# Kernel optimization log

Measured on AMD Instinct MI355X. Metric: run time of the kernel, lower is better.

## Reference

```python
import jax, jax.numpy as jnp
import numpy as np

FILTS = 100  # conv padding = aconv_filts
SCALING = 2.0


def setup_inputs() -> dict:
    key = jax.random.key(0)
    ks = jax.random.split(key, 9)
    T, DUNITS, ATT, EPROJ, CH, K = 50000, 1024, 512, 512, 10, 2 * FILTS + 1
    return {
        "dec_z": jax.random.normal(ks[0], (1, DUNITS), jnp.float32),
        "att_prev": jax.random.uniform(ks[1], (1, T), jnp.float32),
        "pre_compute_enc_h": jax.random.normal(ks[2], (1, T, ATT), jnp.float32),
        "enc_h": jax.random.normal(ks[3], (1, T, EPROJ), jnp.float32),
        "mask": jnp.zeros((1, T), jnp.float32),
        "conv_w": jax.random.normal(ks[4], (CH, 1, K), jnp.float32) * 0.05,
        "w_att": jax.random.normal(ks[5], (ATT, CH), jnp.float32) * 0.05,
        "w_dec": jax.random.normal(ks[6], (ATT, DUNITS), jnp.float32) * 0.02,
        "w_gvec": jax.random.normal(ks[7], (1, ATT), jnp.float32) * 0.05,
        "b_gvec": jnp.zeros((1,), jnp.float32),
    }


def reference(dec_z, att_prev, pre_compute_enc_h, enc_h, mask, conv_w, w_att, w_dec, w_gvec, b_gvec):
    # loc_conv: 1-channel 1D conv over previous attention weights -> [1, CH, T]
    att_conv = jax.lax.conv_general_dilated(
        att_prev[:, None, :], conv_w, window_strides=(1,),
        padding=[(FILTS, FILTS)], dimension_numbers=("NCH", "OIH", "NCH"))
    # mlp_att: [1, T, ATT]
    att_conv = jnp.einsum("bct,ac->bta", att_conv, w_att)
    # mlp_dec, tiled over frames: [1, 1, ATT]
    dec_tiled = (dec_z @ w_dec.T)[:, None, :]
    # gvec(tanh(...)) -> scores e: [1, T]
    e = jnp.einsum("bta,a->bt", jnp.tanh(att_conv + pre_compute_enc_h + dec_tiled), w_gvec[0]) + b_gvec
    e = e + mask
    w = jax.nn.softmax(SCALING * e, axis=1)  # [1, T]
    c = jnp.sum(enc_h * w[..., None], axis=1)  # [1, EPROJ]
    return (c, w)
```

## Files before the change

kernel.cpp:

```cpp
#include <hip/hip_runtime.h>
#include <math.h>


constexpr int ATT    = 512;
constexpr int CH     = 10;
constexpr int KW     = 201;
constexpr int FILTS  = 100;
constexpr int DUNITS = 1024;
constexpr int NB1    = 1024;
constexpr int NB3    = 256;
constexpr float SCALING = 2.0f;

__device__ __forceinline__ float wave_reduce_sum(float v) {
    #pragma unroll
    for (int off = 32; off > 0; off >>= 1) v += __shfl_xor(v, off, 64);
    return v;
}

__device__ __forceinline__ float fast_tanh(float x) {
    x = fminf(fmaxf(x, -15.f), 15.f);
    float e = __expf(2.f * x);
    return __fdividef(e - 1.f, e + 1.f);
}

__global__ __launch_bounds__(256, 4) void k0_conv_dec(
    const float* __restrict__ att_prev,
    const float* __restrict__ conv_w,
    const float* __restrict__ dec_z,
    const float* __restrict__ w_dec,
    float* __restrict__ ws_aconv,
    float* __restrict__ ws_dec,
    int T, int nbconv)
{
    if ((int)blockIdx.x < nbconv) {
        __shared__ float s_ap[256 + KW - 1];
        __shared__ float s_w[CH * KW];
        const int t0 = blockIdx.x * 256;
        for (int i = threadIdx.x; i < 256 + KW - 1; i += 256) {
            int t = t0 - FILTS + i;
            s_ap[i] = (t >= 0 && t < T) ? att_prev[t] : 0.f;
        }
        for (int i = threadIdx.x; i < CH * KW; i += 256) s_w[i] = conv_w[i];
        __syncthreads();
        const int t = t0 + threadIdx.x;
        if (t < T) {
            float acc[CH];
            #pragma unroll
            for (int c = 0; c < CH; ++c) acc[c] = 0.f;
            for (int k = 0; k < KW; ++k) {
                float x = s_ap[threadIdx.x + k];
                #pragma unroll
                for (int c = 0; c < CH; ++c) acc[c] += x * s_w[c * KW + k];
            }
            #pragma unroll
            for (int c = 0; c < CH; ++c) ws_aconv[t * CH + c] = acc[c];
        }
    } else {
        const int b    = blockIdx.x - nbconv;
        const int wid  = threadIdx.x >> 6;
        const int lane = threadIdx.x & 63;
        const int a    = b * 4 + wid;
        const float4* wd = (const float4*)(w_dec + a * DUNITS);
        const float4* dz = (const float4*)dec_z;
        float acc = 0.f;
        #pragma unroll
        for (int q = 0; q < 4; ++q) {
            float4 wv = wd[lane + q * 64];
            float4 zv = dz[lane + q * 64];
            acc += wv.x * zv.x + wv.y * zv.y + wv.z * zv.z + wv.w * zv.w;
        }
        acc = wave_reduce_sum(acc);
        if (lane == 0) ws_dec[a] = acc;
    }
}

__global__ __launch_bounds__(256, 3) void k1_scores(
    const float* __restrict__ pre,
    const float* __restrict__ mask,
    const float* __restrict__ w_att,
    const float* __restrict__ w_gvec,
    const float* __restrict__ b_gvec,
    const float* __restrict__ ws_dec,
    const float* __restrict__ ws_aconv,
    float* __restrict__ ws_e,
    float* __restrict__ ws_ms,
    int T)
{
    __shared__ float s_watt[ATT * CH];
    __shared__ float s_m[4], s_s[4];
    for (int i = threadIdx.x; i < ATT * CH; i += 256) s_watt[i] = w_att[i];
    __syncthreads();

    const int wid  = threadIdx.x >> 6;
    const int lane = threadIdx.x & 63;

    float wa[8][CH];
    #pragma unroll
    for (int j = 0; j < 4; ++j) {
        #pragma unroll
        for (int c = 0; c < CH; ++c) {
            wa[j][c]     = s_watt[(lane * 4 + j) * CH + c];
            wa[4 + j][c] = s_watt[(256 + lane * 4 + j) * CH + c];
        }
    }
    const float4 dlo = ((const float4*)ws_dec)[lane];
    const float4 dhi = ((const float4*)ws_dec)[64 + lane];
    const float4 glo = ((const float4*)w_gvec)[lane];
    const float4 ghi = ((const float4*)w_gvec)[64 + lane];
    const float  bg  = b_gvec[0];

    float m = -INFINITY, s = 0.f;
    const float4* pre4 = (const float4*)pre;
    const int gw = blockIdx.x * 4 + wid;

    for (int tb = gw * 4; tb < T; tb += NB1 * 4 * 4) {
        float4 p0[4], p1[4];
        #pragma unroll
        for (int i = 0; i < 4; ++i) {
            int t = tb + i;
            if (t < T) {
                p0[i] = pre4[t * 128 + lane];
                p1[i] = pre4[t * 128 + 64 + lane];
            }
        }
        #pragma unroll
        for (int i = 0; i < 4; ++i) {
            int t = tb + i;
            if (t >= T) break;
            float ac[CH];
            #pragma unroll
            for (int c = 0; c < CH; ++c) ac[c] = ws_aconv[t * CH + c];
            float av[8];
            #pragma unroll
            for (int j = 0; j < 8; ++j) {
                float v = 0.f;
                #pragma unroll
                for (int c = 0; c < CH; ++c) v += ac[c] * wa[j][c];
                av[j] = v;
            }
            float x0 = fast_tanh(p0[i].x + dlo.x + av[0]);
            float x1 = fast_tanh(p0[i].y + dlo.y + av[1]);
            float x2 = fast_tanh(p0[i].z + dlo.z + av[2]);
            float x3 = fast_tanh(p0[i].w + dlo.w + av[3]);
            float x4 = fast_tanh(p1[i].x + dhi.x + av[4]);
            float x5 = fast_tanh(p1[i].y + dhi.y + av[5]);
            float x6 = fast_tanh(p1[i].z + dhi.z + av[6]);
            float x7 = fast_tanh(p1[i].w + dhi.w + av[7]);
            float acc = glo.x * x0 + glo.y * x1 + glo.z * x2 + glo.w * x3
                      + ghi.x * x4 + ghi.y * x5 + ghi.z * x6 + ghi.w * x7;
            acc = wave_reduce_sum(acc);
            float y = SCALING * (acc + bg + mask[t]);
            if (lane == 0) ws_e[t] = y;
            float nm = fmaxf(m, y);
            s = s * __expf(m - nm) + __expf(y - nm);
            m = nm;
        }
    }
    if (lane == 0) { s_m[wid] = m; s_s[wid] = s; }
    __syncthreads();
    if (threadIdx.x == 0) {
        float M = s_m[0], S = s_s[0];
        #pragma unroll
        for (int w = 1; w < 4; ++w) {
            float m2 = s_m[w], s2 = s_s[w];
            float nm = fmaxf(M, m2);
            S = S * __expf(M - nm) + s2 * __expf(m2 - nm);
            M = nm;
        }
        ws_ms[blockIdx.x * 2]     = M;
        ws_ms[blockIdx.x * 2 + 1] = S;
    }
}

__global__ __launch_bounds__(256, 4) void k2_merge(
    const float* __restrict__ ws_ms, float* __restrict__ ws_glob,
    float* __restrict__ out, int nb)
{
    __shared__ float s_m[256], s_s[256];
    float m = -INFINITY, s = 0.f;
    for (int i = threadIdx.x; i < nb; i += 256) {
        float m2 = ws_ms[i * 2], s2 = ws_ms[i * 2 + 1];
        float nm = fmaxf(m, m2);
        s = s * __expf(m - nm) + s2 * __expf(m2 - nm);
        m = nm;
    }
    s_m[threadIdx.x] = m; s_s[threadIdx.x] = s;
    __syncthreads();
    for (int off = 128; off > 0; off >>= 1) {
        if ((int)threadIdx.x < off) {
            float M = s_m[threadIdx.x], S = s_s[threadIdx.x];
            float m2 = s_m[threadIdx.x + off], s2 = s_s[threadIdx.x + off];
            float nm = fmaxf(M, m2);
            s_s[threadIdx.x] = S * __expf(M - nm) + s2 * __expf(m2 - nm);
            s_m[threadIdx.x] = nm;
        }
        __syncthreads();
    }
    if (threadIdx.x == 0) { ws_glob[0] = s_m[0]; ws_glob[1] = 1.f / s_s[0]; }
    out[threadIdx.x]       = 0.f;
    out[threadIdx.x + 256] = 0.f;
}

__global__ __launch_bounds__(256, 4) void k3_ctx(
    const float* __restrict__ enc_h,
    const float* __restrict__ ws_e,
    const float* __restrict__ ws_glob,
    float* __restrict__ out,
    float* __restrict__ ws_c,
    int T)
{
    const int wid  = threadIdx.x >> 6;
    const int lane = threadIdx.x & 63;
    const float M  = ws_glob[0];
    const float IS = ws_glob[1];
    const float4* eh4 = (const float4*)enc_h;

    float4 a0 = make_float4(0.f, 0.f, 0.f, 0.f);
    float4 a1 = make_float4(0.f, 0.f, 0.f, 0.f);
    const int gw = blockIdx.x * 4 + wid;

    for (int tb = gw * 8; tb < T; tb += NB3 * 4 * 8) {
        float4 e0[8], e1[8];
        float  y[8];
        #pragma unroll
        for (int i = 0; i < 8; ++i) {
            int t = tb + i;
            if (t < T) {
                e0[i] = eh4[t * 128 + lane];
                e1[i] = eh4[t * 128 + 64 + lane];
                y[i]  = ws_e[t];
            }
        }
        #pragma unroll
        for (int i = 0; i < 8; ++i) {
            int t = tb + i;
            if (t >= T) break;
            float w = __expf(y[i] - M) * IS;
            if (lane == 0) out[ATT + t] = w;
            a0.x += w * e0[i].x; a0.y += w * e0[i].y;
            a0.z += w * e0[i].z; a0.w += w * e0[i].w;
            a1.x += w * e1[i].x; a1.y += w * e1[i].y;
            a1.z += w * e1[i].z; a1.w += w * e1[i].w;
        }
    }

    __shared__ float4 s_c[4 * 128];
    s_c[wid * 128 + lane]      = a0;
    s_c[wid * 128 + 64 + lane] = a1;
    __syncthreads();
    const float* sc = (const float*)s_c;
    for (int a = threadIdx.x; a < ATT; a += 256) {
        float v = sc[a] + sc[512 + a] + sc[1024 + a] + sc[1536 + a];
        ws_c[blockIdx.x * ATT + a] = v;
    }
}

__global__ __launch_bounds__(256, 4) void k4_reduce(
    const float* __restrict__ ws_c, float* __restrict__ out)
{
    const int gt  = blockIdx.x * 256 + threadIdx.x;
    const int a   = gt & (ATT - 1);
    const int grp = gt >> 9;
    float v = 0.f;
    #pragma unroll
    for (int i = 0; i < 8; ++i) v += ws_c[(grp * 8 + i) * ATT + a];
    atomicAdd(&out[a], v);
}

extern "C" void kernel_launch(void* const* d_in, const int* in_sizes, int n_in,
                              void* d_out, int out_size, void* d_ws, size_t ws_size,
                              hipStream_t stream)
{
    const float* dec_z    = (const float*)d_in[0];
    const float* att_prev = (const float*)d_in[1];
    const float* pre      = (const float*)d_in[2];
    const float* enc_h    = (const float*)d_in[3];
    const float* mask     = (const float*)d_in[4];
    const float* conv_w   = (const float*)d_in[5];
    const float* w_att    = (const float*)d_in[6];
    const float* w_dec    = (const float*)d_in[7];
    const float* w_gvec   = (const float*)d_in[8];
    const float* b_gvec   = (const float*)d_in[9];
    const int T = in_sizes[1];

    float* ws       = (float*)d_ws;
    float* ws_dec   = ws;
    float* ws_aconv = ws_dec + ATT;
    float* ws_e     = ws_aconv + (size_t)T * CH;
    float* ws_ms    = ws_e + T;
    float* ws_glob  = ws_ms + NB1 * 2;
    float* ws_c     = ws_glob + 4;
    float* out      = (float*)d_out;

    const int nbconv = (T + 255) / 256;

    hipLaunchKernelGGL(k0_conv_dec, dim3(nbconv + ATT / 4), dim3(256), 0, stream,
                       att_prev, conv_w, dec_z, w_dec, ws_aconv, ws_dec, T, nbconv);
    hipLaunchKernelGGL(k1_scores, dim3(NB1), dim3(256), 0, stream,
                       pre, mask, w_att, w_gvec, b_gvec, ws_dec, ws_aconv,
                       ws_e, ws_ms, T);
    hipLaunchKernelGGL(k2_merge, dim3(1), dim3(256), 0, stream,
                       ws_ms, ws_glob, out, NB1);
    hipLaunchKernelGGL(k3_ctx, dim3(NB3), dim3(256), 0, stream,
                       enc_h, ws_e, ws_glob, out, ws_c, T);
    hipLaunchKernelGGL(k4_reduce, dim3(64), dim3(256), 0, stream,
                       ws_c, out);
}
```

Measured before the change: 276.1 us.

## Fold softmax merge and context reduction into ctx kernel, restructure conv

Removes the separate single-block merge kernel by having every ctx block redo the 1024-partial max/sum merge itself. It also drops the final reduce kernel and atomically adds per-block context sums straight into the output. The conv kernel now uses 64-frame tiles, splits the filter taps across four waves and reduces through shared memory. Conv outputs are padded to 12 channels so the scores kernel can load them as float4. The changes cut launch count and serial single-block latency, in exchange for redundant merge work per block and more atomics.

```diff
diff --git a/kernel.cpp b/kernel.cpp
--- a/kernel.cpp
+++ b/kernel.cpp
@@ -4,11 +4,13 @@
 
 constexpr int ATT    = 512;
 constexpr int CH     = 10;
+constexpr int PCH    = 12;
 constexpr int KW     = 201;
 constexpr int FILTS  = 100;
 constexpr int DUNITS = 1024;
 constexpr int NB1    = 1024;
-constexpr int NB3    = 256;
+constexpr int NB3    = 1024;
+constexpr int CT     = 64;
 constexpr float SCALING = 2.0f;
 
 __device__ __forceinline__ float wave_reduce_sum(float v) {
@@ -30,37 +32,59 @@
     const float* __restrict__ w_dec,
     float* __restrict__ ws_aconv,
     float* __restrict__ ws_dec,
+    float* __restrict__ out,
     int T, int nbconv)
 {
     if ((int)blockIdx.x < nbconv) {
-        __shared__ float s_ap[256 + KW - 1];
-        __shared__ float s_w[CH * KW];
-        const int t0 = blockIdx.x * 256;
-        for (int i = threadIdx.x; i < 256 + KW - 1; i += 256) {
+        __shared__ float s_ap[CT + KW - 1];
+        __shared__ float s_wt[KW * 12];
+        __shared__ float s_part[4 * CT * CH];
+        const int t0 = blockIdx.x * CT;
+        for (int i = threadIdx.x; i < CT + KW - 1; i += 256) {
             int t = t0 - FILTS + i;
             s_ap[i] = (t >= 0 && t < T) ? att_prev[t] : 0.f;
         }
-        for (int i = threadIdx.x; i < CH * KW; i += 256) s_w[i] = conv_w[i];
+        for (int i = threadIdx.x; i < CH * KW; i += 256) {
+            int c = i % CH, k = i / CH;
+            s_wt[k * 12 + c] = conv_w[c * KW + k];
+        }
         __syncthreads();
-        const int t = t0 + threadIdx.x;
-        if (t < T) {
-            float acc[CH];
-            #pragma unroll
-            for (int c = 0; c < CH; ++c) acc[c] = 0.f;
-            for (int k = 0; k < KW; ++k) {
-                float x = s_ap[threadIdx.x + k];
-                #pragma unroll
-                for (int c = 0; c < CH; ++c) acc[c] += x * s_w[c * KW + k];
-            }
-            #pragma unroll
-            for (int c = 0; c < CH; ++c) ws_aconv[t * CH + c] = acc[c];
+        const int tl = threadIdx.x & 63;
+        const int kq = threadIdx.x >> 6;
+        float acc[CH];
+        #pragma unroll
+        for (int c = 0; c < CH; ++c) acc[c] = 0.f;
+        for (int k = kq; k < KW; k += 4) {
+            float x = s_ap[tl + k];
+            const float4 w0 = *(const float4*)&s_wt[k * 12];
+            const float4 w1 = *(const float4*)&s_wt[k * 12 + 4];
+            const float2 w2 = *(const float2*)&s_wt[k * 12 + 8];
+            acc[0] += x * w0.x; acc[1] += x * w0.y;
+            acc[2] += x * w0.z; acc[3] += x * w0.w;
+            acc[4] += x * w1.x; acc[5] += x * w1.y;
+            acc[6] += x * w1.z; acc[7] += x * w1.w;
+            acc[8] += x * w2.x; acc[9] += x * w2.y;
+        }
+        #pragma unroll
+        for (int c = 0; c < CH; ++c) s_part[kq * (CT * CH) + tl * CH + c] = acc[c];
+        __syncthreads();
+        for (int idx = threadIdx.x; idx < CT * PCH; idx += 256) {
+            int t = idx / PCH, c = idx % PCH;
+            float v = 0.f;
+            if (c < CH) {
+                int j = t * CH + c;
+                v = s_part[j] + s_part[CT * CH + j]
+                  + s_part[2 * CT * CH + j] + s_part[3 * CT * CH + j];
+            }
+            if (t0 + t < T) ws_aconv[(size_t)(t0 + t) * PCH + c] = v;
         }
     } else {
         const int b    = blockIdx.x - nbconv;
         const int wid  = threadIdx.x >> 6;
         const int lane = threadIdx.x & 63;
         const int a    = b * 4 + wid;
-        const float4* wd = (const float4*)(w_dec + a * DUNITS);
+        if (threadIdx.x < 4) out[b * 4 + threadIdx.x] = 0.f;
+        const float4* wd = (const float4*)(w_dec + (size_t)a * DUNITS);
         const float4* dz = (const float4*)dec_z;
         float acc = 0.f;
         #pragma unroll
@@ -111,25 +135,29 @@
 
     float m = -INFINITY, s = 0.f;
     const float4* pre4 = (const float4*)pre;
+    const float4* ac4  = (const float4*)ws_aconv;
     const int gw = blockIdx.x * 4 + wid;
 
     for (int tb = gw * 4; tb < T; tb += NB1 * 4 * 4) {
         float4 p0[4], p1[4];
+        float  msk[4];
         #pragma unroll
         for (int i = 0; i < 4; ++i) {
             int t = tb + i;
             if (t < T) {
-                p0[i] = pre4[t * 128 + lane];
-                p1[i] = pre4[t * 128 + 64 + lane];
+                p0[i]  = pre4[(size_t)t * 128 + lane];
+                p1[i]  = pre4[(size_t)t * 128 + 64 + lane];
+                msk[i] = mask[t];
             }
         }
         #pragma unroll
         for (int i = 0; i < 4; ++i) {
             int t = tb + i;
             if (t >= T) break;
-            float ac[CH];
-            #pragma unroll
-            for (int c = 0; c < CH; ++c) ac[c] = ws_aconv[t * CH + c];
+            float ac[12];
+            *(float4*)&ac[0] = ac4[(size_t)t * 3 + 0];
+            *(float4*)&ac[4] = ac4[(size_t)t * 3 + 1];
+            *(float4*)&ac[8] = ac4[(size_t)t * 3 + 2];
             float av[8];
             #pragma unroll
             for (int j = 0; j < 8; ++j) {
@@ -149,7 +177,7 @@
             float acc = glo.x * x0 + glo.y * x1 + glo.z * x2 + glo.w * x3
                       + ghi.x * x4 + ghi.y * x5 + ghi.z * x6 + ghi.w * x7;
             acc = wave_reduce_sum(acc);
-            float y = SCALING * (acc + bg + mask[t]);
+            float y = SCALING * (acc + bg + msk[i]);
             if (lane == 0) ws_e[t] = y;
             float nm = fmaxf(m, y);
             s = s * __expf(m - nm) + __expf(y - nm);
@@ -172,67 +200,60 @@
     }
 }
 
-__global__ __launch_bounds__(256, 4) void k2_merge(
-    const float* __restrict__ ws_ms, float* __restrict__ ws_glob,
-    float* __restrict__ out, int nb)
-{
-    __shared__ float s_m[256], s_s[256];
-    float m = -INFINITY, s = 0.f;
-    for (int i = threadIdx.x; i < nb; i += 256) {
-        float m2 = ws_ms[i * 2], s2 = ws_ms[i * 2 + 1];
-        float nm = fmaxf(m, m2);
-        s = s * __expf(m - nm) + s2 * __expf(m2 - nm);
-        m = nm;
-    }
-    s_m[threadIdx.x] = m; s_s[threadIdx.x] = s;
-    __syncthreads();
-    for (int off = 128; off > 0; off >>= 1) {
-        if ((int)threadIdx.x < off) {
-            float M = s_m[threadIdx.x], S = s_s[threadIdx.x];
-            float m2 = s_m[threadIdx.x + off], s2 = s_s[threadIdx.x + off];
-            float nm = fmaxf(M, m2);
-            s_s[threadIdx.x] = S * __expf(M - nm) + s2 * __expf(m2 - nm);
-            s_m[threadIdx.x] = nm;
-        }
-        __syncthreads();
-    }
-    if (threadIdx.x == 0) { ws_glob[0] = s_m[0]; ws_glob[1] = 1.f / s_s[0]; }
-    out[threadIdx.x]       = 0.f;
-    out[threadIdx.x + 256] = 0.f;
-}
-
 __global__ __launch_bounds__(256, 4) void k3_ctx(
     const float* __restrict__ enc_h,
     const float* __restrict__ ws_e,
-    const float* __restrict__ ws_glob,
+    const float* __restrict__ ws_ms,
     float* __restrict__ out,
-    float* __restrict__ ws_c,
     int T)
 {
+    __shared__ float s_m[256], s_s[256];
+    {
+        float m = -INFINITY, s = 0.f;
+        for (int i = threadIdx.x; i < NB1; i += 256) {
+            float m2 = ws_ms[i * 2], s2 = ws_ms[i * 2 + 1];
+            float nm = fmaxf(m, m2);
+            s = s * __expf(m - nm) + s2 * __expf(m2 - nm);
+            m = nm;
+        }
+        s_m[threadIdx.x] = m; s_s[threadIdx.x] = s;
+        __syncthreads();
+        for (int off = 128; off > 0; off >>= 1) {
+            if ((int)threadIdx.x < off) {
+                float M = s_m[threadIdx.x], S = s_s[threadIdx.x];
+                float m2 = s_m[threadIdx.x + off], s2 = s_s[threadIdx.x + off];
+                float nm = fmaxf(M, m2);
+                s_s[threadIdx.x] = S * __expf(M - nm) + s2 * __expf(m2 - nm);
+                s_m[threadIdx.x] = nm;
+            }
+            __syncthreads();
+        }
+    }
+    const float M  = s_m[0];
+    const float IS = 1.f / s_s[0];
+
     const int wid  = threadIdx.x >> 6;
     const int lane = threadIdx.x & 63;
-    const float M  = ws_glob[0];
-    const float IS = ws_glob[1];
     const float4* eh4 = (const float4*)enc_h;
 
     float4 a0 = make_float4(0.f, 0.f, 0.f, 0.f);
     float4 a1 = make_float4(0.f, 0.f, 0.f, 0.f);
     const int gw = blockIdx.x * 4 + wid;
 
-    for (int tb = gw * 8; tb < T; tb += NB3 * 4 * 8) {
-        float4 e0[8], e1[8];
-        float  y[8];
-        #pragma unroll
-        for (int i = 0; i < 8; ++i) {
+    for (int tb = gw * 4; tb < T; tb += NB3 * 4 * 4) {
+        float4 e0[4], e1[4];
+        float  y[4];
+        #pragma unroll
+        for (int i = 0; i < 4; ++i) {
             int t = tb + i;
             if (t < T) {
-                e0[i] = eh4[t * 128 + lane];
-                e1[i] = eh4[t * 128 + 64 + lane];
+                e0[i] = eh4[(size_t)t * 128 + lane];
+                e1[i] = eh4[(size_t)t * 128 + 64 + lane];
                 y[i]  = ws_e[t];
             }
         }
         #pragma unroll
-        for (int i = 0; i < 8; ++i) {
+        for (int i = 0; i < 4; ++i) {
             int t = tb + i;
             if (t >= T) break;
             float w = __expf(y[i] - M) * IS;
@@ -251,20 +272,8 @@
     const float* sc = (const float*)s_c;
     for (int a = threadIdx.x; a < ATT; a += 256) {
         float v = sc[a] + sc[512 + a] + sc[1024 + a] + sc[1536 + a];
-        ws_c[blockIdx.x * ATT + a] = v;
-    }
-}
-
-__global__ __launch_bounds__(256, 4) void k4_reduce(
-    const float* __restrict__ ws_c, float* __restrict__ out)
-{
-    const int gt  = blockIdx.x * 256 + threadIdx.x;
-    const int a   = gt & (ATT - 1);
-    const int grp = gt >> 9;
-    float v = 0.f;
-    #pragma unroll
-    for (int i = 0; i < 8; ++i) v += ws_c[(grp * 8 + i) * ATT + a];
-    atomicAdd(&out[a], v);
+        atomicAdd(&out[a], v);
+    }
 }
 
 extern "C" void kernel_launch(void* const* d_in, const int* in_sizes, int n_in,
@@ -286,23 +295,17 @@
     float* ws       = (float*)d_ws;
     float* ws_dec   = ws;
     float* ws_aconv = ws_dec + ATT;
-    float* ws_e     = ws_aconv + (size_t)T * CH;
+    float* ws_e     = ws_aconv + (size_t)T * PCH;
     float* ws_ms    = ws_e + T;
-    float* ws_glob  = ws_ms + NB1 * 2;
-    float* ws_c     = ws_glob + 4;
     float* out      = (float*)d_out;
 
-    const int nbconv = (T + 255) / 256;
+    const int nbconv = (T + CT - 1) / CT;
 
     hipLaunchKernelGGL(k0_conv_dec, dim3(nbconv + ATT / 4), dim3(256), 0, stream,
-                       att_prev, conv_w, dec_z, w_dec, ws_aconv, ws_dec, T, nbconv);
+                       att_prev, conv_w, dec_z, w_dec, ws_aconv, ws_dec, out, T, nbconv);
     hipLaunchKernelGGL(k1_scores, dim3(NB1), dim3(256), 0, stream,
                        pre, mask, w_att, w_gvec, b_gvec, ws_dec, ws_aconv,
                        ws_e, ws_ms, T);
-    hipLaunchKernelGGL(k2_merge, dim3(1), dim3(256), 0, stream,
-                       ws_ms, ws_glob, out, NB1);
     hipLaunchKernelGGL(k3_ctx, dim3(NB3), dim3(256), 0, stream,
-                       enc_h, ws_e, ws_glob, out, ws_c, T);
-    hipLaunchKernelGGL(k4_reduce, dim3(64), dim3(256), 0, stream,
-                       ws_c, out);
-}
+                       enc_h, ws_e, ws_ms, out, T);
+}
```

After: 273.5 us. Within noise of the previous version (-0.9%).
